# Performance work log

Hardware: AMD Instinct MI355X
Metric: run time of the kernel (lower is better)

## Reference

```python
import jax, jax.numpy as jnp
import numpy as np

D_MODEL = 3072
N_HEADS = 24
HEAD_DIM = D_MODEL // N_HEADS          # 128
Q_PROJ = D_MODEL // 2                  # 1536
KV_PROJ = 2 * D_MODEL // 3             # 2048
ROPE_DIM = HEAD_DIM // 2               # 64 (qk_rope_dim == qk_no_rope_dim)
MAX_LEN = 2048
ROPE_THETA = 10000.0
EPS = 1e-6
B, S = 2, 2048


def setup_inputs() -> dict:
    key = jax.random.key(0)
    ks = jax.random.split(key, 7)
    return {
        "x": jax.random.normal(ks[0], (B, S, D_MODEL), dtype=jnp.float32),
        "scale": jnp.ones((D_MODEL,), dtype=jnp.float32),
        "w_dq": 0.01 * jax.random.normal(ks[1], (D_MODEL, Q_PROJ), dtype=jnp.float32),
        "w_uq": 0.01 * jax.random.normal(ks[2], (Q_PROJ, D_MODEL), dtype=jnp.float32),
        "w_dkv": 0.01 * jax.random.normal(ks[3], (D_MODEL, KV_PROJ + ROPE_DIM), dtype=jnp.float32),
        "w_ukv": 0.01 * jax.random.normal(ks[4], (KV_PROJ, D_MODEL + N_HEADS * ROPE_DIM), dtype=jnp.float32),
        "w_o": 0.01 * jax.random.normal(ks[5], (D_MODEL, D_MODEL), dtype=jnp.float32),
    }


def _rope_cos_sin(seq_len):
    # freqs over full head_dim, sliced to rope_dim//2 then tiled x2 (as in torch repeat)
    freqs = 1.0 / (ROPE_THETA ** (jnp.arange(0, HEAD_DIM, 2, dtype=jnp.float32) / HEAD_DIM))
    angles = jnp.arange(seq_len, dtype=jnp.float32)[:, None] * freqs[None, :]  # [S, 64]
    ang = angles[:, : ROPE_DIM // 2]                                            # [S, 32]
    cos = jnp.tile(jnp.cos(ang), (1, 2))                                        # [S, 64]
    sin = jnp.tile(jnp.sin(ang), (1, 2))
    return cos[None, None], sin[None, None]  # [1,1,S,64]


def _rotate_half(t):
    a, b = jnp.split(t, 2, axis=-1)
    return jnp.concatenate([-b, a], axis=-1)


def reference(x, scale, w_dq, w_uq, w_dkv, w_ukv, w_o):
    b, s, _ = x.shape
    # RMSNorm pre-normalization
    xn = scale * (x * jax.lax.rsqrt(jnp.mean(x * x, axis=-1, keepdims=True) + EPS))
    # two-stage query projection
    q = (xn @ w_dq) @ w_uq                                   # [B,S,D]
    q = q.reshape(b, s, N_HEADS, HEAD_DIM).transpose(0, 2, 1, 3)  # [B,H,S,hd]
    q_no_rope, q_rope = jnp.split(q, [ROPE_DIM], axis=-1)
    cos, sin = _rope_cos_sin(s)
    q_rope = q_rope * cos + _rotate_half(q_rope) * sin
    # KV down projection (this is the kv cache)
    kv_down = xn @ w_dkv                                     # [B,S,KV_PROJ+rope]
    kv_no_rope, k_rope = jnp.split(kv_down, [KV_PROJ], axis=-1)
    # KV up projection
    kv_up = kv_no_rope @ w_ukv                               # [B,S,H*(hd+rope)]
    kv_up = kv_up.reshape(b, s, N_HEADS, HEAD_DIM + ROPE_DIM).transpose(0, 2, 1, 3)
    key, value = jnp.split(kv_up, [ROPE_DIM], axis=-1)       # key [B,H,S,64], value [B,H,S,128]
    # shared rope key (one head, broadcast to all heads)
    k_rope = k_rope[:, None, :, :]                           # [B,1,S,64]
    k_rope = k_rope * cos + _rotate_half(k_rope) * sin
    k_rope = jnp.broadcast_to(k_rope, (b, N_HEADS, s, ROPE_DIM))
    final_q = jnp.concatenate([q_no_rope, q_rope], axis=-1)  # [B,H,S,128]
    final_k = jnp.concatenate([key, k_rope], axis=-1)        # [B,H,S,128]
    # masked SDPA (causal, past_length=0)
    inv_scale = 1.0 / jnp.sqrt(jnp.asarray(HEAD_DIM, dtype=x.dtype))
    scores = jnp.einsum("bhsd,bhtd->bhst", final_q, final_k) * inv_scale
    causal = jnp.tril(jnp.ones((s, s), dtype=bool))
    scores = jnp.where(causal[None, None], scores, jnp.asarray(-1e30, dtype=scores.dtype))
    attn = jax.nn.softmax(scores, axis=-1)
    attn_out = jnp.einsum("bhst,bhtd->bhsd", attn, value)    # [B,H,S,128]
    attn_out = attn_out.transpose(0, 2, 1, 3).reshape(b, s, D_MODEL)
    output = attn_out @ w_o.T
    return output, kv_down
```

## Files before the change

kernel.cpp:

```cpp
#include <hip/hip_runtime.h>
#include <hip/hip_bf16.h>
#include <stdint.h>

using bf16_t = __bf16;
using bf16x8 = __attribute__((ext_vector_type(8))) __bf16;
using bf16x4 = __attribute__((ext_vector_type(4))) __bf16;
using f32x4  = __attribute__((ext_vector_type(4))) float;

#define D_MODEL 3072
#define N_HEADS 24
#define HEAD_DIM 128
#define Q_PROJ 1536
#define KV_PROJ 2048
#define ROPE_DIM 64
#define S_LEN 2048
#define NTOK 4096
#define KVDN 2112
#define KVUN 4608

__device__ __forceinline__ void async_ld16(const void* g, void* l) {
    __builtin_amdgcn_global_load_lds(
        (__attribute__((address_space(1))) uint32_t*)(uintptr_t)g,
        (__attribute__((address_space(3))) uint32_t*)(uint32_t)(uintptr_t)l,
        16, 0, 0);
}

#define BARRIER() __builtin_amdgcn_s_barrier()
#define WAITV4() asm volatile("s_waitcnt vmcnt(4)" ::: "memory")
#define WAITV0() asm volatile("s_waitcnt vmcnt(0)" ::: "memory")
#define LGKM0()  do { asm volatile("s_waitcnt lgkmcnt(0)" ::: "memory"); \
                      __builtin_amdgcn_sched_barrier(0); } while (0)

__global__ __launch_bounds__(256) void rmsnorm_kernel(
    const float* __restrict__ x, const float* __restrict__ sc, bf16_t* __restrict__ xn)
{
    const int tok = blockIdx.x;
    const int t = threadIdx.x;
    const float4* xr = (const float4*)(x + (size_t)tok * D_MODEL);
    float4 a = xr[t], b = xr[t + 256], c = xr[t + 512];
    float ss = a.x*a.x + a.y*a.y + a.z*a.z + a.w*a.w
             + b.x*b.x + b.y*b.y + b.z*b.z + b.w*b.w
             + c.x*c.x + c.y*c.y + c.z*c.z + c.w*c.w;
    #pragma unroll
    for (int off = 32; off >= 1; off >>= 1) ss += __shfl_xor(ss, off);
    __shared__ float red[4];
    if ((t & 63) == 0) red[t >> 6] = ss;
    __syncthreads();
    const float inv = rsqrtf((red[0] + red[1] + red[2] + red[3]) * (1.0f / D_MODEL) + 1e-6f);
    const float4* sr = (const float4*)sc;
    float4 s0 = sr[t], s1 = sr[t + 256], s2 = sr[t + 512];
    bf16x4* xo = (bf16x4*)(xn + (size_t)tok * D_MODEL);
    bf16x4 o;
    o[0]=(bf16_t)(a.x*s0.x*inv); o[1]=(bf16_t)(a.y*s0.y*inv); o[2]=(bf16_t)(a.z*s0.z*inv); o[3]=(bf16_t)(a.w*s0.w*inv);
    xo[t] = o;
    o[0]=(bf16_t)(b.x*s1.x*inv); o[1]=(bf16_t)(b.y*s1.y*inv); o[2]=(bf16_t)(b.z*s1.z*inv); o[3]=(bf16_t)(b.w*s1.w*inv);
    xo[t + 256] = o;
    o[0]=(bf16_t)(c.x*s2.x*inv); o[1]=(bf16_t)(c.y*s2.y*inv); o[2]=(bf16_t)(c.z*s2.z*inv); o[3]=(bf16_t)(c.w*s2.w*inv);
    xo[t + 512] = o;
}

__global__ void transpose_conv(const float* __restrict__ in, bf16_t* __restrict__ out, int K, int N)
{
    __shared__ float tile[32][33];
    const int n0 = blockIdx.x * 32, k0 = blockIdx.y * 32;
    const int tx = threadIdx.x, ty = threadIdx.y;
    #pragma unroll
    for (int i = 0; i < 32; i += 8)
        tile[ty + i][tx] = in[(size_t)(k0 + ty + i) * N + n0 + tx];
    __syncthreads();
    #pragma unroll
    for (int i = 0; i < 32; i += 8)
        out[(size_t)(n0 + ty + i) * K + k0 + tx] = (bf16_t)tile[tx][ty + i];
}

__global__ void conv_bf16(const float* __restrict__ in, bf16_t* __restrict__ out, int n4)
{
    const int stride = gridDim.x * 256;
    for (int i = blockIdx.x * 256 + threadIdx.x; i < n4; i += stride) {
        float4 v = ((const float4*)in)[i];
        bf16x4 o;
        o[0] = (bf16_t)v.x; o[1] = (bf16_t)v.y; o[2] = (bf16_t)v.z; o[3] = (bf16_t)v.w;
        ((bf16x4*)out)[i] = o;
    }
}

template<int RH>
__device__ __forceinline__ void mfma16(f32x4 (&acc)[8][4], const bf16x8 (&af)[4],
                                       const bf16x8 (&bfv)[4]) {
    __builtin_amdgcn_s_setprio(1);
    #pragma unroll
    for (int i = 0; i < 4; ++i)
        #pragma unroll
        for (int cf = 0; cf < 4; ++cf)
            acc[RH*4+i][cf] = __builtin_amdgcn_mfma_f32_16x16x32_bf16(af[i], bfv[cf], acc[RH*4+i][cf], 0, 0, 0);
    __builtin_amdgcn_s_setprio(0);
}

__global__ __launch_bounds__(512, 2) void gemm256(
    const bf16_t* __restrict__ A, const bf16_t* __restrict__ B, int N, int K,
    float* __restrict__ Cf, int ldf, int flo, int fhi,
    bf16_t* __restrict__ Cb1, int ldb1, int b1lo, int b1hi,
    bf16_t* __restrict__ Cb2, int ldb2, int b2lo, int b2hi)
{
    __shared__ char LDS[131072];
    char* Lc = LDS;
    const int tid = threadIdx.x;
    const int wv = tid >> 6, lane = tid & 63;
    const int fr = lane & 15, fg = lane >> 4;
    const int wr = wv >> 2, wc = wv & 3;

    int lin = blockIdx.y * gridDim.x + blockIdx.x;
    const int nwg = gridDim.x * gridDim.y;
    if ((nwg & 7) == 0) lin = (lin & 7) * (nwg >> 3) + (lin >> 3);
    const int bx = lin % gridDim.x, by = lin / gridDim.x;
    const int m0 = by << 8, n0 = bx << 8;

    const uint32_t slot4 = (uint32_t)((fg ^ ((fr >> 1) & 3)) << 4);

    int grow[2], gcol[2];
    const bf16_t* agp[2]; const bf16_t* bgp[2];
    uint32_t aoff[2], boff[2];
    #pragma unroll
    for (int j = 0; j < 2; ++j) {
        const int c = j * 512 + tid;
        const int g = c ^ ((c >> 3) & 3);
        grow[j] = g >> 2; gcol[j] = g & 3;
        agp[j] = A + (size_t)(m0 + grow[j]) * K + gcol[j] * 8;
        int br = n0 + grow[j]; if (br > N - 1) br = N - 1;
        bgp[j] = B + (size_t)br * K + gcol[j] * 8;
        aoff[j] = (uint32_t)((j * 8 + wv) * 1024);
        boff[j] = (uint32_t)(65536 + (j * 8 + wv) * 1024);
    }

    f32x4 acc[8][4];
    f32x4 zero = {0.f, 0.f, 0.f, 0.f};
    #pragma unroll
    for (int i = 0; i < 8; ++i)
        #pragma unroll
        for (int j = 0; j < 4; ++j) acc[i][j] = zero;

    bf16x8 af[4], bfv[4];
    const int rowA = (wr << 7) + fr;
    const int rowB = (wc << 6) + fr;

    auto stA = [&](int t, int kh) {
        const uint32_t sb = (uint32_t)(((2*t + kh) & 3) << 14);
        #pragma unroll
        for (int j = 0; j < 2; ++j)
            async_ld16(agp[j] + t * 64 + kh * 32, Lc + sb + aoff[j]);
    };
    auto stB = [&](int t, int kh) {
        const uint32_t sb = (uint32_t)(((2*t + kh) & 3) << 14);
        #pragma unroll
        for (int j = 0; j < 2; ++j)
            async_ld16(bgp[j] + t * 64 + kh * 32, Lc + sb + boff[j]);
    };
    auto ldA4 = [&](int t, int kh, int rh) {
        const uint32_t base = (uint32_t)(((2*t + kh) & 3) << 14);
        #pragma unroll
        for (int i = 0; i < 4; ++i)
            af[i] = *(const bf16x8*)(Lc + base + (rowA + (rh * 4 + i) * 16) * 64 + slot4);
    };
    auto ldB4 = [&](int t, int kh) {
        const uint32_t base = (uint32_t)(65536 + (((2*t + kh) & 3) << 14));
        #pragma unroll
        for (int cf = 0; cf < 4; ++cf)
            bfv[cf] = *(const bf16x8*)(Lc + base + (rowB + cf * 16) * 64 + slot4);
    };

    const int NT = K >> 6;
    stA(0, 0); stB(0, 0); stA(0, 1); stB(0, 1);
    WAITV4(); BARRIER();

    for (int t = 0; t < NT; ++t) {
        const bool pref = (t < NT - 1);
        ldA4(t, 0, 0); ldB4(t, 0); if (pref) stA(t + 1, 0);
        BARRIER(); LGKM0();
        mfma16<0>(acc, af, bfv);
        BARRIER();
        ldA4(t, 0, 1); if (pref) stB(t + 1, 0);
        if (pref) { WAITV4(); } else { WAITV0(); }
        BARRIER(); LGKM0();
        mfma16<1>(acc, af, bfv);
        BARRIER();
        ldA4(t, 1, 0); ldB4(t, 1); if (pref) stA(t + 1, 1);
        BARRIER(); LGKM0();
        mfma16<0>(acc, af, bfv);
        BARRIER();
        ldA4(t, 1, 1); if (pref) stB(t + 1, 1);
        WAITV4();
        BARRIER(); LGKM0();
        mfma16<1>(acc, af, bfv);
        BARRIER();
    }

    const int colb = n0 + (wc << 6) + fr;
    const int rowb = m0 + (wr << 7) + fg * 4;
    #pragma unroll
    for (int rf = 0; rf < 8; ++rf)
        #pragma unroll
        for (int cf = 0; cf < 4; ++cf) {
            const int col = colb + cf * 16;
            #pragma unroll
            for (int r = 0; r < 4; ++r) {
                const int row = rowb + rf * 16 + r;
                const float v = acc[rf][cf][r];
                if (Cf  && col >= flo  && col < fhi)  Cf [(size_t)row * ldf  + col - flo]  = v;
                if (Cb1 && col >= b1lo && col < b1hi) Cb1[(size_t)row * ldb1 + col - b1lo] = (bf16_t)v;
                if (Cb2 && col >= b2lo && col < b2hi) Cb2[(size_t)row * ldb2 + col - b2lo] = (bf16_t)v;
            }
        }
}

__global__ void rope_tab(float* __restrict__ ctab, float* __restrict__ stab)
{
    const int idx = blockIdx.x * 256 + threadIdx.x;
    if (idx >= S_LEN * 32) return;
    const int s = idx >> 5, i = idx & 31;
    const float freq = powf(10000.0f, -(float)(2 * i) * (1.0f / 128.0f));
    const float ang = (float)s * freq;
    ctab[idx] = cosf(ang);
    stab[idx] = sinf(ang);
}

__global__ void rope_q_kernel(bf16_t* __restrict__ q, const float* __restrict__ ctab,
                              const float* __restrict__ stab)
{
    const int idx = blockIdx.x * 256 + threadIdx.x;
    if (idx >= NTOK * N_HEADS * 32) return;
    const int i = idx & 31;
    const int rest = idx >> 5;
    const int h = rest % N_HEADS;
    const int tok = rest / N_HEADS;
    const int s = tok & (S_LEN - 1);
    bf16_t* p = q + (size_t)tok * D_MODEL + h * HEAD_DIM + 64;
    const float a = (float)p[i], b = (float)p[i + 32];
    const float c = ctab[s * 32 + i], sn = stab[s * 32 + i];
    p[i]      = (bf16_t)(a * c - b * sn);
    p[i + 32] = (bf16_t)(b * c + a * sn);
}

__global__ void rope_k_kernel(const float* __restrict__ kvd, bf16_t* __restrict__ kr,
                              const float* __restrict__ ctab, const float* __restrict__ stab)
{
    const int idx = blockIdx.x * 256 + threadIdx.x;
    if (idx >= NTOK * 32) return;
    const int i = idx & 31;
    const int tok = idx >> 5;
    const int s = tok & (S_LEN - 1);
    const float* p = kvd + (size_t)tok * KVDN + KV_PROJ;
    const float a = p[i], b = p[i + 32];
    const float c = ctab[s * 32 + i], sn = stab[s * 32 + i];
    kr[(size_t)tok * 64 + i]      = (bf16_t)(a * c - b * sn);
    kr[(size_t)tok * 64 + i + 32] = (bf16_t)(b * c + a * sn);
}

__global__ void vt_asm(const bf16_t* __restrict__ kvup, bf16_t* __restrict__ vt)
{
    __shared__ bf16_t tile[32][33];
    const int s0 = blockIdx.x * 32, d0 = blockIdx.y * 32, bh = blockIdx.z;
    const int b = bh / N_HEADS, h = bh % N_HEADS;
    const int tx = threadIdx.x, ty = threadIdx.y;
    #pragma unroll
    for (int i = 0; i < 32; i += 8)
        tile[ty + i][tx] = kvup[(size_t)(b * S_LEN + s0 + ty + i) * KVUN + h * 192 + 64 + d0 + tx];
    __syncthreads();
    #pragma unroll
    for (int i = 0; i < 32; i += 8)
        vt[((size_t)bh * HEAD_DIM + d0 + ty + i) * S_LEN + s0 + tx] = tile[tx][ty + i];
}

__global__ __launch_bounds__(256, 2) void attn_fwd(
    const bf16_t* __restrict__ Q, const bf16_t* __restrict__ KVUP,
    const bf16_t* __restrict__ KR, const bf16_t* __restrict__ VT,
    bf16_t* __restrict__ AO)
{
    __shared__ bf16_t Knr[2][64 * 64];
    __shared__ bf16_t Krp[2][64 * 64];
    __shared__ bf16_t Vls[2][128 * 64];

    const int bh = blockIdx.y;
    const int b = bh / N_HEADS, h = bh % N_HEADS;
    const int wave = threadIdx.x >> 6, lane = threadIdx.x & 63;
    const int fr = lane & 15, fg = lane >> 4;
    const int rx = fr & 7;
    const int hi = fg >> 1;
    const int s0l = fr + 32 * (fg & 1);
    const int s1l = s0l + 16;

    const bf16_t* Kb  = KVUP + (size_t)b * S_LEN * KVUN + (size_t)h * 192;
    const bf16_t* KRb = KR + (size_t)b * S_LEN * 64;
    const bf16_t* Vb  = VT + (size_t)bh * HEAD_DIM * S_LEN;

    const int srow   = lane >> 3;
    const int schunk = (lane & 7) ^ srow;
    const float l2e_isc = 0.127500625f;

    f32x4 zero = {0.f, 0.f, 0.f, 0.f};

    #pragma unroll 1
    for (int tp = 0; tp < 2; ++tp) {
        const int qt = (tp == 0) ? blockIdx.x : (15 - blockIdx.x);
        const int qb = qt * 128;
        const int wrow0 = qb + wave * 32;

        bf16x8 qf[2][4];
        #pragma unroll
        for (int rf = 0; rf < 2; ++rf)
            #pragma unroll
            for (int kc = 0; kc < 4; ++kc)
                qf[rf][kc] = *(const bf16x8*)(Q + (size_t)(b * S_LEN + wrow0 + rf * 16 + fr) * D_MODEL
                                              + h * HEAD_DIM + kc * 32 + fg * 8);
        f32x4 oacc[2][8];
        float m_i[2], l_i[2];
        #pragma unroll
        for (int rf = 0; rf < 2; ++rf) {
            #pragma unroll
            for (int nf = 0; nf < 8; ++nf) oacc[rf][nf] = zero;
            m_i[rf] = -1e30f; l_i[rf] = 0.f;
        }

        auto stage = [&](int kvb, int bf) {
            #pragma unroll
            for (int c = 0; c < 2; ++c) {
                const int r0 = wave * 16 + c * 8;
                async_ld16(Kb  + (size_t)(kvb + r0 + srow) * KVUN + schunk * 8, &Knr[bf][r0 * 64]);
                async_ld16(KRb + (size_t)(kvb + r0 + srow) * 64   + schunk * 8, &Krp[bf][r0 * 64]);
            }
            #pragma unroll
            for (int c = 0; c < 4; ++c) {
                const int r0 = wave * 32 + c * 8;
                async_ld16(Vb + (size_t)(r0 + srow) * S_LEN + kvb + schunk * 8, &Vls[bf][r0 * 64]);
            }
        };

        const int kvend = qb + 128;
        int cur = 0;
        stage(0, 0);
        __syncthreads();

        #pragma unroll 1
        for (int kvb = 0; kvb < kvend; kvb += 64) {
            if (kvb + 64 < kvend) stage(kvb + 64, cur ^ 1);

            if (kvb <= wrow0 + 31) {
                const bf16_t* Kc = Knr[cur];
                const bf16_t* Rc = Krp[cur];
                const bf16_t* Vc = Vls[cur];

                f32x4 sacc[2][4];
                #pragma unroll
                for (int rf = 0; rf < 2; ++rf)
                    #pragma unroll
                    for (int jn = 0; jn < 4; ++jn) sacc[rf][jn] = zero;
                __builtin_amdgcn_s_setprio(1);
                #pragma unroll
                for (int jn = 0; jn < 4; ++jn) {
                    const int krow = jn * 16 + fr;
                    bf16x8 kA = *(const bf16x8*)(Kc + krow * 64 + (((0 + fg) ^ rx) << 3));
                    bf16x8 kB = *(const bf16x8*)(Kc + krow * 64 + (((4 + fg) ^ rx) << 3));
                    bf16x8 kC = *(const bf16x8*)(Rc + krow * 64 + (((0 + fg) ^ rx) << 3));
                    bf16x8 kD = *(const bf16x8*)(Rc + krow * 64 + (((4 + fg) ^ rx) << 3));
                    #pragma unroll
                    for (int rf = 0; rf < 2; ++rf) {
                        sacc[rf][jn] = __builtin_amdgcn_mfma_f32_16x16x32_bf16(kA, qf[rf][0], sacc[rf][jn], 0, 0, 0);
                        sacc[rf][jn] = __builtin_amdgcn_mfma_f32_16x16x32_bf16(kB, qf[rf][1], sacc[rf][jn], 0, 0, 0);
                        sacc[rf][jn] = __builtin_amdgcn_mfma_f32_16x16x32_bf16(kC, qf[rf][2], sacc[rf][jn], 0, 0, 0);
                        sacc[rf][jn] = __builtin_amdgcn_mfma_f32_16x16x32_bf16(kD, qf[rf][3], sacc[rf][jn], 0, 0, 0);
                    }
                }
                __builtin_amdgcn_s_setprio(0);

                const bool needMask = (kvb + 63 > wrow0);
                uint32_t pk[2][4][2];
                float scf[2];
                #pragma unroll
                for (int rf = 0; rf < 2; ++rf) {
                    const int qrow = wrow0 + rf * 16 + fr;
                    float mx = -1e30f;
                    #pragma unroll
                    for (int jn = 0; jn < 4; ++jn)
                        #pragma unroll
                        for (int r = 0; r < 4; ++r) {
                            float v = sacc[rf][jn][r] * l2e_isc;
                            if (needMask && (kvb + jn * 16 + fg * 4 + r > qrow)) v = -1e30f;
                            sacc[rf][jn][r] = v;
                            mx = fmaxf(mx, v);
                        }
                    mx = fmaxf(mx, __shfl_xor(mx, 16));
                    mx = fmaxf(mx, __shfl_xor(mx, 32));
                    const float mn = fmaxf(m_i[rf], mx);
                    scf[rf] = __builtin_amdgcn_exp2f(m_i[rf] - mn);
                    m_i[rf] = mn;
                    float ls = 0.f;
                    #pragma unroll
                    for (int jn = 0; jn < 4; ++jn) {
                        float p0 = __builtin_amdgcn_exp2f(sacc[rf][jn][0] - mn);
                        float p1 = __builtin_amdgcn_exp2f(sacc[rf][jn][1] - mn);
                        float p2 = __builtin_amdgcn_exp2f(sacc[rf][jn][2] - mn);
                        float p3 = __builtin_amdgcn_exp2f(sacc[rf][jn][3] - mn);
                        ls += (p0 + p1) + (p2 + p3);
                        union { bf16x4 h; uint32_t w[2]; } cv;
                        cv.h[0] = (bf16_t)p0; cv.h[1] = (bf16_t)p1;
                        cv.h[2] = (bf16_t)p2; cv.h[3] = (bf16_t)p3;
                        pk[rf][jn][0] = cv.w[0]; pk[rf][jn][1] = cv.w[1];
                    }
                    ls += __shfl_xor(ls, 16);
                    ls += __shfl_xor(ls, 32);
                    l_i[rf] = l_i[rf] * scf[rf] + ls;
                    #pragma unroll
                    for (int nf = 0; nf < 8; ++nf)
                        #pragma unroll
                        for (int r = 0; r < 4; ++r) oacc[rf][nf][r] *= scf[rf];
                }

                bf16x8 bfr[2][2];
                #pragma unroll
                for (int rf = 0; rf < 2; ++rf)
                    #pragma unroll
                    for (int ks = 0; ks < 2; ++ks) {
                        const uint32_t t00 = __shfl(pk[rf][2*ks][0],   s0l);
                        const uint32_t t01 = __shfl(pk[rf][2*ks][1],   s0l);
                        const uint32_t t10 = __shfl(pk[rf][2*ks+1][0], s0l);
                        const uint32_t t11 = __shfl(pk[rf][2*ks+1][1], s0l);
                        const uint32_t u00 = __shfl(pk[rf][2*ks][0],   s1l);
                        const uint32_t u01 = __shfl(pk[rf][2*ks][1],   s1l);
                        const uint32_t u10 = __shfl(pk[rf][2*ks+1][0], s1l);
                        const uint32_t u11 = __shfl(pk[rf][2*ks+1][1], s1l);
                        union { bf16x8 h; uint32_t w[4]; } bb;
                        bb.w[0] = hi ? t10 : t00;
                        bb.w[1] = hi ? t11 : t01;
                        bb.w[2] = hi ? u10 : u00;
                        bb.w[3] = hi ? u11 : u01;
                        bfr[rf][ks] = bb.h;
                    }

                __builtin_amdgcn_s_setprio(1);
                #pragma unroll
                for (int nf = 0; nf < 8; ++nf) {
                    const int vrow = nf * 16 + fr;
                    bf16x8 v0 = *(const bf16x8*)(Vc + vrow * 64 + (((0 + fg) ^ rx) << 3));
                    bf16x8 v1 = *(const bf16x8*)(Vc + vrow * 64 + (((4 + fg) ^ rx) << 3));
                    #pragma unroll
                    for (int rf = 0; rf < 2; ++rf) {
                        oacc[rf][nf] = __builtin_amdgcn_mfma_f32_16x16x32_bf16(v0, bfr[rf][0], oacc[rf][nf], 0, 0, 0);
                        oacc[rf][nf] = __builtin_amdgcn_mfma_f32_16x16x32_bf16(v1, bfr[rf][1], oacc[rf][nf], 0, 0, 0);
                    }
                }
                __builtin_amdgcn_s_setprio(0);
            }
            __syncthreads();
            cur ^= 1;
        }

        #pragma unroll
        for (int rf = 0; rf < 2; ++rf) {
            const float rl = __builtin_amdgcn_rcpf(l_i[rf]);
            const int qrow = wrow0 + rf * 16 + fr;
            bf16_t* aob = AO + (size_t)(b * S_LEN + qrow) * D_MODEL + h * HEAD_DIM + fg * 4;
            #pragma unroll
            for (int nf = 0; nf < 8; ++nf) {
                bf16x4 o;
                o[0] = (bf16_t)(oacc[rf][nf][0] * rl);
                o[1] = (bf16_t)(oacc[rf][nf][1] * rl);
                o[2] = (bf16_t)(oacc[rf][nf][2] * rl);
                o[3] = (bf16_t)(oacc[rf][nf][3] * rl);
                *(bf16x4*)(aob + nf * 16) = o;
            }
        }
    }
}

extern "C" void kernel_launch(void* const* d_in, const int* in_sizes, int n_in,
                              void* d_out, int out_size, void* d_ws, size_t ws_size,
                              hipStream_t stream)
{
    const float* x     = (const float*)d_in[0];
    const float* scale = (const float*)d_in[1];
    const float* w_dq  = (const float*)d_in[2];
    const float* w_uq  = (const float*)d_in[3];
    const float* w_dkv = (const float*)d_in[4];
    const float* w_ukv = (const float*)d_in[5];
    const float* w_o   = (const float*)d_in[6];
    float* out0 = (float*)d_out;
    float* out1 = out0 + (size_t)NTOK * D_MODEL;

    if (ws_size < 187039744ull) return;
    char* ws = (char*)d_ws;
    bf16_t* XN    = (bf16_t*)(ws + 0);
    bf16_t* WCAT  = (bf16_t*)(ws + 25165824ull);
    bf16_t* WUQT  = (bf16_t*)(ws + 47579136ull);
    bf16_t* WUKVT = (bf16_t*)(ws + 57016320ull);
    bf16_t* WOB   = (bf16_t*)(ws + 75890688ull);
    bf16_t* QD    = (bf16_t*)(ws + 94765056ull);
    bf16_t* Qb    = (bf16_t*)(ws + 107347968ull);
    bf16_t* KVNR  = (bf16_t*)(ws + 132513792ull);
    bf16_t* KVUP  = (bf16_t*)(ws + 149291008ull);
    bf16_t* KRB   = (bf16_t*)(ws + 94765056ull);
    float*  CTAB  = (float*) (ws + 95289344ull);
    float*  STAB  = (float*) (ws + 95551488ull);
    bf16_t* VTb   = WCAT;
    bf16_t* AO    = XN;

    rmsnorm_kernel<<<NTOK, 256, 0, stream>>>(x, scale, XN);
    transpose_conv<<<dim3(1536/32, 3072/32), dim3(32,8), 0, stream>>>(w_dq,  WCAT, 3072, 1536);
    transpose_conv<<<dim3(2112/32, 3072/32), dim3(32,8), 0, stream>>>(w_dkv, WCAT + (size_t)1536*3072, 3072, 2112);
    transpose_conv<<<dim3(3072/32, 1536/32), dim3(32,8), 0, stream>>>(w_uq,  WUQT, 1536, 3072);
    transpose_conv<<<dim3(4608/32, 2048/32), dim3(32,8), 0, stream>>>(w_ukv, WUKVT, 2048, 4608);
    conv_bf16<<<2048, 256, 0, stream>>>(w_o, WOB, (D_MODEL * D_MODEL) / 4);

    gemm256<<<dim3(15, 16), 512, 0, stream>>>(XN, WCAT, 3648, 3072,
        out1, KVDN, 1536, 3648,
        QD,   Q_PROJ, 0, 1536,
        KVNR, KV_PROJ, 1536, 3584);
    gemm256<<<dim3(12, 16), 512, 0, stream>>>(QD, WUQT, 3072, 1536,
        nullptr, 0, 0, 0, Qb, D_MODEL, 0, 3072, nullptr, 0, 0, 0);
    rope_tab<<<(S_LEN * 32 + 255) / 256, 256, 0, stream>>>(CTAB, STAB);
    rope_q_kernel<<<(NTOK * N_HEADS * 32 + 255) / 256, 256, 0, stream>>>(Qb, CTAB, STAB);
    rope_k_kernel<<<(NTOK * 32 + 255) / 256, 256, 0, stream>>>(out1, KRB, CTAB, STAB);
    gemm256<<<dim3(18, 16), 512, 0, stream>>>(KVNR, WUKVT, 4608, 2048,
        nullptr, 0, 0, 0, KVUP, KVUN, 0, 4608, nullptr, 0, 0, 0);
    vt_asm<<<dim3(S_LEN/32, HEAD_DIM/32, 48), dim3(32,8), 0, stream>>>(KVUP, VTb);
    attn_fwd<<<dim3(8, 48), 256, 0, stream>>>(Qb, KVUP, KRB, VTb, AO);
    gemm256<<<dim3(12, 16), 512, 0, stream>>>(AO, WOB, 3072, 3072,
        out0, D_MODEL, 0, 3072, nullptr, 0, 0, 0, nullptr, 0, 0, 0);
}
```

Measured before the change: 563.3 us.

## Double-buffer GEMM fragment registers to overlap LDS reads with MFMA

Replaces the single fragment register set with ping-pong A/B register buffers, so the LDS fragment loads for the next sub-step are issued before the current MFMA block runs. It removes the explicit lgkmcnt waits and about half the barriers in the K loop, and reorders the global-to-LDS prefetches so each half-tile is issued together, with a vmcnt(0) wait once per tile. The cost is higher register pressure from the extra fragment sets. There is also a risk of LDS buffer hazards, because stage-buffer reuse now relies on fewer barriers and a coarser wait.

```diff
diff --git a/kernel.cpp b/kernel.cpp
--- a/kernel.cpp
+++ b/kernel.cpp
@@ -26,10 +26,7 @@
 }
 
 #define BARRIER() __builtin_amdgcn_s_barrier()
-#define WAITV4() asm volatile("s_waitcnt vmcnt(4)" ::: "memory")
 #define WAITV0() asm volatile("s_waitcnt vmcnt(0)" ::: "memory")
-#define LGKM0()  do { asm volatile("s_waitcnt lgkmcnt(0)" ::: "memory"); \
-                      __builtin_amdgcn_sched_barrier(0); } while (0)
 
 __global__ __launch_bounds__(256) void rmsnorm_kernel(
     const float* __restrict__ x, const float* __restrict__ sc, bf16_t* __restrict__ xn)
@@ -139,7 +136,7 @@
         #pragma unroll
         for (int j = 0; j < 4; ++j) acc[i][j] = zero;
 
-    bf16x8 af[4], bfv[4];
+    bf16x8 A0[4], A1[4], B0[4], B1[4];
     const int rowA = (wr << 7) + fr;
     const int rowB = (wc << 6) + fr;
 
@@ -155,42 +152,40 @@
         for (int j = 0; j < 2; ++j)
             async_ld16(bgp[j] + t * 64 + kh * 32, Lc + sb + boff[j]);
     };
-    auto ldA4 = [&](int t, int kh, int rh) {
+    auto ldA4 = [&](int t, int kh, int rh, bf16x8 (&dst)[4]) {
         const uint32_t base = (uint32_t)(((2*t + kh) & 3) << 14);
         #pragma unroll
         for (int i = 0; i < 4; ++i)
-            af[i] = *(const bf16x8*)(Lc + base + (rowA + (rh * 4 + i) * 16) * 64 + slot4);
+            dst[i] = *(const bf16x8*)(Lc + base + (rowA + (rh * 4 + i) * 16) * 64 + slot4);
     };
-    auto ldB4 = [&](int t, int kh) {
+    auto ldB4 = [&](int t, int kh, bf16x8 (&dst)[4]) {
         const uint32_t base = (uint32_t)(65536 + (((2*t + kh) & 3) << 14));
         #pragma unroll
         for (int cf = 0; cf < 4; ++cf)
-            bfv[cf] = *(const bf16x8*)(Lc + base + (rowB + cf * 16) * 64 + slot4);
+            dst[cf] = *(const bf16x8*)(Lc + base + (rowB + cf * 16) * 64 + slot4);
     };
 
     const int NT = K >> 6;
     stA(0, 0); stB(0, 0); stA(0, 1); stB(0, 1);
-    WAITV4(); BARRIER();
+    WAITV0(); BARRIER();
+    ldA4(0, 0, 0, A0); ldB4(0, 0, B0);
 
     for (int t = 0; t < NT; ++t) {
         const bool pref = (t < NT - 1);
-        ldA4(t, 0, 0); ldB4(t, 0); if (pref) stA(t + 1, 0);
-        BARRIER(); LGKM0();
-        mfma16<0>(acc, af, bfv);
+        ldA4(t, 0, 1, A1);
+        if (pref) { stA(t + 1, 0); stB(t + 1, 0); }
+        mfma16<0>(acc, A0, B0);
         BARRIER();
-        ldA4(t, 0, 1); if (pref) stB(t + 1, 0);
-        if (pref) { WAITV4(); } else { WAITV0(); }
-        BARRIER(); LGKM0();
-        mfma16<1>(acc, af, bfv);
+        ldA4(t, 1, 0, A0); ldB4(t, 1, B1);
+        if (pref) { stA(t + 1, 1); stB(t + 1, 1); }
+        mfma16<1>(acc, A1, B0);
         BARRIER();
-        ldA4(t, 1, 0); ldB4(t, 1); if (pref) stA(t + 1, 1);
-        BARRIER(); LGKM0();
-        mfma16<0>(acc, af, bfv);
+        ldA4(t, 1, 1, A1);
+        mfma16<0>(acc, A0, B1);
+        if (pref) WAITV0();
         BARRIER();
-        ldA4(t, 1, 1); if (pref) stB(t + 1, 1);
-        WAITV4();
-        BARRIER(); LGKM0();
-        mfma16<1>(acc, af, bfv);
+        if (pref) { ldA4(t + 1, 0, 0, A0); ldB4(t + 1, 0, B0); }
+        mfma16<1>(acc, A1, B1);
         BARRIER();
     }
 
```

Measured after the change: 570.2 us. No clear change (+1.2%).
